# Optimization experiments

Hardware: AMD Instinct MI355X
Metric: run time of the kernel (lower is better)

The kernel has to match this reference:

```python
import jax, jax.numpy as jnp
import numpy as np
import math

EMBED_DIM = 1024
NUM_HEADS = 16
HEAD_DIM = EMBED_DIM // NUM_HEADS  # 64
MAX_SEQ_LEN = 2048


def rope_tables(max_seq_len, dim):
    pos = jnp.arange(max_seq_len, dtype=jnp.float32)
    div_term = jnp.exp(jnp.arange(0, dim, 2, dtype=jnp.float32) * -(math.log(10000.0) / dim))
    ang = pos[:, None] * div_term[None, :]  # [S, dim//2]
    return jnp.sin(ang), jnp.cos(ang)


def apply_rope(x, sin, cos):
    # x: [B, H, S, D]; sin/cos: [max_seq, D//2]
    S = x.shape[2]
    sin = sin[:S][None, None]  # [1,1,S,D//2]
    cos = cos[:S][None, None]
    x1, x2 = jnp.split(x, 2, axis=-1)
    return jnp.concatenate([cos * x1 - sin * x2, sin * x1 + cos * x2], axis=-1)


def setup_inputs() -> dict:
    key = jax.random.key(0)
    ks = jax.random.split(key, 5)
    B, S, E = 4, 2048, EMBED_DIM
    std = 1.0 / math.sqrt(E)
    x = jax.random.normal(ks[0], (B, S, E), dtype=jnp.float32)
    Wq = jax.random.normal(ks[1], (E, E), dtype=jnp.float32) * std
    Wk = jax.random.normal(ks[2], (E, E), dtype=jnp.float32) * std
    Wv = jax.random.normal(ks[3], (E, E), dtype=jnp.float32) * std
    Wo = jax.random.normal(ks[4], (E, E), dtype=jnp.float32) * std
    return {"x": x, "Wq": Wq, "Wk": Wk, "Wv": Wv, "Wo": Wo}


def reference(x, Wq, Wk, Wv, Wo):
    B, S, E = x.shape
    H, D = NUM_HEADS, HEAD_DIM
    scale = 1.0 / math.sqrt(D)
    sin, cos = rope_tables(MAX_SEQ_LEN, D)

    def split_heads(t):
        return t.reshape(B, S, H, D).transpose(0, 2, 1, 3)  # [B,H,S,D]

    q = split_heads(x @ Wq)
    k = split_heads(x @ Wk)
    v = split_heads(x @ Wv)
    q = apply_rope(q, sin, cos)
    k = apply_rope(k, sin, cos)

    scores = jnp.einsum('bhqd,bhkd->bhqk', q, k) * scale
    causal = jnp.where(jnp.tril(jnp.ones((S, S), dtype=bool)), 0.0, -1e9)
    scores = scores + causal[None, None]
    attn = jax.nn.softmax(scores, axis=-1)
    out = jnp.einsum('bhqk,bhkd->bhqd', attn, v)  # [B,H,S,D]
    out = out.transpose(0, 2, 1, 3).reshape(B, S, E)
    return out @ Wo
```

## Files before the change

### kernel.cpp

```cpp
#include <hip/hip_runtime.h>

#define DEVFN __device__ __forceinline__

typedef __attribute__((ext_vector_type(8))) short bf16x8;
typedef __attribute__((ext_vector_type(4))) float f32x4;
typedef __attribute__((ext_vector_type(16))) float f32x16;

#define MFMA16(a, b, c) __builtin_amdgcn_mfma_f32_16x16x32_bf16(a, b, c, 0, 0, 0)
#define MFMA32(a, b, c) __builtin_amdgcn_mfma_f32_32x32x16_bf16(a, b, c, 0, 0, 0)

DEVFN unsigned short f2bf(float f) {
  union { float f; unsigned u; } v; v.f = f;
  unsigned r = v.u + 0x7FFFu + ((v.u >> 16) & 1u);
  return (unsigned short)(r >> 16);
}
DEVFN unsigned pack2bf(float a, float b) {
  return (unsigned)f2bf(a) | ((unsigned)f2bf(b) << 16);
}
DEVFN unsigned cvtpk(float lo, float hi) {
  unsigned r;
  asm("v_cvt_pk_bf16_f32 %0, %1, %2" : "=v"(r) : "v"(lo), "v"(hi));
  return r;
}
DEVFN void pl32swap(unsigned& a, unsigned& b) {
  asm("v_permlane32_swap_b32 %0, %1" : "+v"(a), "+v"(b));
}
DEVFN void gll16(const void* g, void* l) {
  __builtin_amdgcn_global_load_lds((__attribute__((address_space(1))) void*)g,
                                   (__attribute__((address_space(3))) void*)l,
                                   16, 0, 0);
}


__global__ __launch_bounds__(256) void conv_x_k(const float* __restrict__ x,
                                                unsigned short* __restrict__ xb) {
  int i = (blockIdx.x * 256 + threadIdx.x) * 4;
  float4 v = *(const float4*)(x + i);
  uint2 u;
  u.x = pack2bf(v.x, v.y);
  u.y = pack2bf(v.z, v.w);
  *(uint2*)(xb + i) = u;
}

__global__ __launch_bounds__(256) void transp_k(
    const float* __restrict__ Wq, const float* __restrict__ Wk,
    const float* __restrict__ Wv, const float* __restrict__ Wo,
    unsigned short* __restrict__ Tq, unsigned short* __restrict__ Tk,
    unsigned short* __restrict__ Tv, unsigned short* __restrict__ To) {
  __shared__ unsigned short t[64 * 65];
  int z = blockIdx.z;
  const float* src = (z == 0) ? Wq : (z == 1) ? Wk : (z == 2) ? Wv : Wo;
  unsigned short* dst = (z == 0) ? Tq : (z == 1) ? Tk : (z == 2) ? Tv : To;
  int k0 = blockIdx.x * 64, n0 = blockIdx.y * 64;
  int tid = threadIdx.x;
#pragma unroll
  for (int i = 0; i < 16; ++i) {
    int flat = i * 256 + tid;
    int r = flat >> 6, cc = flat & 63;
    t[cc * 65 + r] = f2bf(src[(size_t)(k0 + r) * 1024 + n0 + cc]);
  }
  __syncthreads();
#pragma unroll
  for (int i = 0; i < 16; ++i) {
    int flat = i * 256 + tid;
    int rr = flat >> 6, cc = flat & 63;
    dst[(size_t)(n0 + rr) * 1024 + k0 + cc] = t[rr * 65 + cc];
  }
}

__global__ __launch_bounds__(256) void rope_k(float2* __restrict__ rtab) {
  int idx = blockIdx.x * 256 + threadIdx.x;
  int s = idx >> 5, j = idx & 31;
  float freq = expf(-0.28782313714981824f * (float)j);
  float ang = (float)s * freq;
  rtab[idx] = make_float2(sinf(ang), cosf(ang));
}

__global__ __launch_bounds__(256) void gemm_qkv_k(
    const unsigned short* __restrict__ A, const unsigned short* __restrict__ WTq,
    const unsigned short* __restrict__ WTk, const unsigned short* __restrict__ WTv,
    unsigned short* __restrict__ Qb, unsigned short* __restrict__ Kfb,
    unsigned short* __restrict__ Vfb, const float2* __restrict__ rtab) {
  __shared__ unsigned short At[128 * 64];
  __shared__ unsigned short Bt[128 * 64];
  const int tid = threadIdx.x;
  const int w = tid >> 6, lane = tid & 63, g = lane >> 4, c = lane & 15;
  const int wr = w >> 1, wc = w & 1;
  const int which = blockIdx.y >> 3;
  const unsigned short* WT = (which == 0) ? WTq : (which == 1) ? WTk : WTv;
  const int m0 = blockIdx.x * 128, n0 = (blockIdx.y & 7) * 128;

  f32x4 zero = {0.f, 0.f, 0.f, 0.f};
  f32x4 acc[4][4];
#pragma unroll
  for (int i = 0; i < 4; ++i)
#pragma unroll
    for (int j = 0; j < 4; ++j) acc[i][j] = zero;

  for (int k0 = 0; k0 < 1024; k0 += 64) {
#pragma unroll
    for (int p = 0; p < 4; ++p) {
      int i = p * 256 + tid;
      int row = i >> 3, ls = i & 7;
      size_t off = ((size_t)(m0 + row) * 1024 + k0) * 2 + ((ls ^ (row & 7)) << 4);
      gll16((const char*)A + off, (char*)At + p * 4096 + w * 1024);
      size_t offb = ((size_t)(n0 + row) * 1024 + k0) * 2 + ((ls ^ (row & 7)) << 4);
      gll16((const char*)WT + offb, (char*)Bt + p * 4096 + w * 1024);
    }
    __syncthreads();
#pragma unroll
    for (int ks = 0; ks < 2; ++ks) {
      bf16x8 af[4], bfv[4];
#pragma unroll
      for (int am = 0; am < 4; ++am) {
        int row = wr * 64 + am * 16 + c;
        af[am] = *(const bf16x8*)(At + row * 64 + ((((ks << 2) | g) ^ (row & 7)) << 3));
      }
#pragma unroll
      for (int bn = 0; bn < 4; ++bn) {
        int row = wc * 64 + bn * 16 + c;
        bfv[bn] = *(const bf16x8*)(Bt + row * 64 + ((((ks << 2) | g) ^ (row & 7)) << 3));
      }
#pragma unroll
      for (int am = 0; am < 4; ++am)
#pragma unroll
        for (int bn = 0; bn < 4; ++bn)
          acc[am][bn] = MFMA16(af[am], bfv[bn], acc[am][bn]);
    }
    __syncthreads();
  }

  if (which == 0) {
#pragma unroll
    for (int am = 0; am < 4; ++am)
#pragma unroll
      for (int bp = 0; bp < 2; ++bp) {
        int col = n0 + wc * 64 + bp * 16 + c;
        int h = col >> 6, j = col & 63;
#pragma unroll
        for (int r = 0; r < 4; ++r) {
          int row = m0 + wr * 64 + am * 16 + (g << 2) + r;
          int b = row >> 11, s = row & 2047;
          float x1 = acc[am][bp][r], x2 = acc[am][bp + 2][r];
          float2 sc = rtab[s * 32 + j];
          float o1 = (sc.y * x1 - sc.x * x2) * 0.18033688011112042f;
          float o2 = (sc.x * x1 + sc.y * x2) * 0.18033688011112042f;
          size_t base = (((size_t)(b * 16 + h)) * 2048 + s) * 64;
          Qb[base + j] = f2bf(o1);
          Qb[base + 32 + j] = f2bf(o2);
        }
      }
  } else if (which == 1) {
#pragma unroll
    for (int am = 0; am < 4; ++am)
#pragma unroll
      for (int bp = 0; bp < 2; ++bp) {
        int col = n0 + wc * 64 + bp * 16 + c;
        int h = col >> 6, j = col & 63;
        const int kb = j >> 4, hil = (j >> 3) & 1, el = j & 7;
#pragma unroll
        for (int r = 0; r < 4; ++r) {
          int row = m0 + wr * 64 + am * 16 + (g << 2) + r;
          int b = row >> 11, s = row & 2047;
          float x1 = acc[am][bp][r], x2 = acc[am][bp + 2][r];
          float2 sc = rtab[s * 32 + j];
          float o1 = sc.y * x1 - sc.x * x2;
          float o2 = sc.x * x1 + sc.y * x2;
          size_t base = (size_t)(b * 16 + h) * 131072 + (size_t)(s >> 5) * 2048 +
                        (hil * 32 + (s & 31)) * 8 + el;
          Kfb[base + kb * 512] = f2bf(o1);
          Kfb[base + (kb + 2) * 512] = f2bf(o2);
        }
      }
  } else {
#pragma unroll
    for (int am = 0; am < 4; ++am)
#pragma unroll
      for (int bn = 0; bn < 4; ++bn) {
        int col = n0 + wc * 64 + bn * 16 + c;
        int h = col >> 6, d = col & 63;
        int row0 = m0 + wr * 64 + am * 16 + (g << 2);
        int b = row0 >> 11, s0 = row0 & 2047;
        uint2 u;
        u.x = pack2bf(acc[am][bn][0], acc[am][bn][1]);
        u.y = pack2bf(acc[am][bn][2], acc[am][bn][3]);
        size_t off = (size_t)(b * 16 + h) * 131072 + (size_t)(s0 >> 6) * 4096 +
                     ((s0 >> 4) & 3) * 1024 + (d >> 5) * 512 +
                     (((s0 >> 3) & 1) * 32 + (d & 31)) * 8 + (s0 & 7);
        *(uint2*)(Vfb + off) = u;
      }
  }
}

__global__ __launch_bounds__(256) void gemm_o_k(
    const unsigned short* __restrict__ A, const unsigned short* __restrict__ WT,
    float* __restrict__ outf) {
  __shared__ unsigned short At[128 * 64];
  __shared__ unsigned short Bt[128 * 64];
  const int tid = threadIdx.x;
  const int w = tid >> 6, lane = tid & 63, g = lane >> 4, c = lane & 15;
  const int wr = w >> 1, wc = w & 1;
  const int m0 = blockIdx.x * 128, n0 = blockIdx.y * 128;

  f32x4 zero = {0.f, 0.f, 0.f, 0.f};
  f32x4 acc[4][4];
#pragma unroll
  for (int i = 0; i < 4; ++i)
#pragma unroll
    for (int j = 0; j < 4; ++j) acc[i][j] = zero;

  for (int k0 = 0; k0 < 1024; k0 += 64) {
#pragma unroll
    for (int p = 0; p < 4; ++p) {
      int i = p * 256 + tid;
      int row = i >> 3, ls = i & 7;
      size_t off = ((size_t)(m0 + row) * 1024 + k0) * 2 + ((ls ^ (row & 7)) << 4);
      gll16((const char*)A + off, (char*)At + p * 4096 + w * 1024);
      size_t offb = ((size_t)(n0 + row) * 1024 + k0) * 2 + ((ls ^ (row & 7)) << 4);
      gll16((const char*)WT + offb, (char*)Bt + p * 4096 + w * 1024);
    }
    __syncthreads();
#pragma unroll
    for (int ks = 0; ks < 2; ++ks) {
      bf16x8 af[4], bfv[4];
#pragma unroll
      for (int am = 0; am < 4; ++am) {
        int row = wr * 64 + am * 16 + c;
        af[am] = *(const bf16x8*)(At + row * 64 + ((((ks << 2) | g) ^ (row & 7)) << 3));
      }
#pragma unroll
      for (int bn = 0; bn < 4; ++bn) {
        int row = wc * 64 + bn * 16 + c;
        bfv[bn] = *(const bf16x8*)(Bt + row * 64 + ((((ks << 2) | g) ^ (row & 7)) << 3));
      }
#pragma unroll
      for (int am = 0; am < 4; ++am)
#pragma unroll
        for (int bn = 0; bn < 4; ++bn)
          acc[am][bn] = MFMA16(af[am], bfv[bn], acc[am][bn]);
    }
    __syncthreads();
  }

#pragma unroll
  for (int am = 0; am < 4; ++am)
#pragma unroll
    for (int bn = 0; bn < 4; ++bn)
#pragma unroll
      for (int r = 0; r < 4; ++r)
        outf[(size_t)(m0 + wr * 64 + am * 16 + (g << 2) + r) * 1024 +
             (n0 + wc * 64 + bn * 16 + c)] = acc[am][bn][r];
}

__global__ __launch_bounds__(256, 2) void attn_k(
    const unsigned short* __restrict__ Q, const unsigned short* __restrict__ Kf,
    const unsigned short* __restrict__ Vf, unsigned short* __restrict__ ctx) {
  const int blk = blockIdx.x;
  const int xcd = blk & 7, j = blk >> 3;
  const int hp = j & 3;
  const int s = 31 - (j >> 2);
  const int tid = threadIdx.x;
  const int w = tid >> 6, lane = tid & 63;
  const int hi = lane >> 5, c5 = lane & 31;
  const int bh = xcd * 8 + hp * 2 + (w & 1);
  const int U = 2 * s + (w >> 1);
  const int S = s + 1;
  const int qw = U * 32;

  const unsigned short* Qbh = Q + (size_t)bh * 2048 * 64;
  const unsigned short* Kbh = Kf + (size_t)bh * 131072;
  const unsigned short* Vbh = Vf + (size_t)bh * 131072;
  const int b = bh >> 4, h = bh & 15;

  f32x16 zacc;
#pragma unroll
  for (int i = 0; i < 16; ++i) zacc[i] = 0.f;

  bf16x8 qf[4];
#pragma unroll
  for (int kb = 0; kb < 4; ++kb)
    qf[kb] = *(const bf16x8*)(Qbh + (size_t)(qw + c5) * 64 + kb * 16 + hi * 8);

  f32x16 oacc[2];
  oacc[0] = zacc; oacc[1] = zacc;
  float m_run = -1e30f, l_run = 0.f;

  bf16x8 kfA[2][4], vfA[2][4], kfB[2][4], vfB[2][4];

  auto loadK = [&](int st, bf16x8 (&dst)[2][4]) {
    const unsigned short* kb_ = Kbh + (size_t)st * 4096 + lane * 8;
#pragma unroll
    for (int t = 0; t < 2; ++t)
#pragma unroll
      for (int kb = 0; kb < 4; ++kb)
        dst[t][kb] = *(const bf16x8*)(kb_ + t * 2048 + kb * 512);
  };
  auto loadV = [&](int st, bf16x8 (&dst)[2][4]) {
    const unsigned short* vb_ = Vbh + (size_t)st * 4096 + lane * 8;
#pragma unroll
    for (int kb = 0; kb < 4; ++kb) {
      dst[0][kb] = *(const bf16x8*)(vb_ + kb * 1024);
      dst[1][kb] = *(const bf16x8*)(vb_ + kb * 1024 + 512);
    }
  };

  auto step = [&](int st, bf16x8 (&kfC)[2][4], bf16x8 (&vfC)[2][4],
                  bf16x8 (&kfN)[2][4], bf16x8 (&vfN)[2][4]) {
    f32x16 sacc[2];
    __builtin_amdgcn_s_setprio(1);
#pragma unroll
    for (int t = 0; t < 2; ++t) {
      sacc[t] = MFMA32(kfC[t][0], qf[0], zacc);
#pragma unroll
      for (int kb = 1; kb < 4; ++kb)
        sacc[t] = MFMA32(kfC[t][kb], qf[kb], sacc[t]);
    }
    __builtin_amdgcn_s_setprio(0);

    if (st + 1 < S) {
      loadK(st + 1, kfN);
      loadV(st + 1, vfN);
    }

    if (st == S - 1) {
      const int q = qw + c5;
#pragma unroll
      for (int t = 0; t < 2; ++t) {
        const int kvb = st * 64 + t * 32 + (hi << 2);
#pragma unroll
        for (int i = 0; i < 16; ++i) {
          int kv = kvb + (i & 3) + ((i >> 2) << 3);
          if (kv > q) sacc[t][i] = -1e30f;
        }
      }
    }

    float vmax = fmaxf(sacc[0][0], sacc[0][1]);
#pragma unroll
    for (int t = 0; t < 2; ++t)
#pragma unroll
      for (int i = (t == 0 ? 2 : 0); i < 16; i += 2)
        vmax = fmaxf(vmax, fmaxf(sacc[t][i], sacc[t][i + 1]));
    vmax = fmaxf(vmax, __shfl_xor(vmax, 32, 64));
    if (!__all(vmax <= m_run + 8.0f)) {
      float m_new = fmaxf(m_run, vmax);
      float alpha = exp2f(m_run - m_new);
      l_run *= alpha;
#pragma unroll
      for (int i = 0; i < 16; ++i) {
        oacc[0][i] *= alpha;
        oacc[1][i] *= alpha;
      }
      m_run = m_new;
    }
    float psum = 0.f;
#pragma unroll
    for (int t = 0; t < 2; ++t)
#pragma unroll
      for (int i = 0; i < 16; ++i) {
        float pv = exp2f(sacc[t][i] - m_run);
        sacc[t][i] = pv;
        psum += pv;
      }
    psum += __shfl_xor(psum, 32, 64);
    l_run += psum;

    unsigned pword[4][4];
#pragma unroll
    for (int t = 0; t < 2; ++t) {
      unsigned X[4][2];
#pragma unroll
      for (int u2 = 0; u2 < 4; ++u2)
#pragma unroll
        for (int wp = 0; wp < 2; ++wp)
          X[u2][wp] = cvtpk(sacc[t][u2 * 4 + 2 * wp], sacc[t][u2 * 4 + 2 * wp + 1]);
#pragma unroll
      for (int par = 0; par < 2; ++par) {
        const int kb = 2 * t + par;
#pragma unroll
        for (int wp = 0; wp < 2; ++wp) {
          unsigned a = X[2 * par][wp], b2 = X[2 * par + 1][wp];
          pl32swap(a, b2);
          pword[kb][wp] = a;
          pword[kb][wp + 2] = b2;
        }
      }
    }

    __builtin_amdgcn_s_setprio(1);
#pragma unroll
    for (int kb = 0; kb < 4; ++kb) {
      union { unsigned u[4]; bf16x8 v; } pw;
#pragma unroll
      for (int k2 = 0; k2 < 4; ++k2) pw.u[k2] = pword[kb][k2];
      oacc[0] = MFMA32(vfC[0][kb], pw.v, oacc[0]);
      oacc[1] = MFMA32(vfC[1][kb], pw.v, oacc[1]);
    }
    __builtin_amdgcn_s_setprio(0);
  };

  loadK(0, kfA);
  loadV(0, vfA);
  for (int st = 0; st < S; st += 2) {
    step(st, kfA, vfA, kfB, vfB);
    if (st + 1 < S) step(st + 1, kfB, vfB, kfA, vfA);
  }

  const float linv = 1.f / l_run;
  unsigned short* crow = ctx + ((size_t)(b * 2048 + qw + c5)) * 1024 + h * 64;
#pragma unroll
  for (int dt = 0; dt < 2; ++dt)
#pragma unroll
    for (int u = 0; u < 4; ++u) {
      int d0 = dt * 32 + 8 * u + 4 * hi;
      uint2 o;
      o.x = cvtpk(oacc[dt][4 * u] * linv, oacc[dt][4 * u + 1] * linv);
      o.y = cvtpk(oacc[dt][4 * u + 2] * linv, oacc[dt][4 * u + 3] * linv);
      *(uint2*)(crow + d0) = o;
    }
}


extern "C" void kernel_launch(void* const* d_in, const int* in_sizes, int n_in,
                              void* d_out, int out_size, void* d_ws, size_t ws_size,
                              hipStream_t stream) {
  (void)in_sizes; (void)n_in; (void)out_size; (void)ws_size;
  const float* x = (const float*)d_in[0];
  const float* Wq = (const float*)d_in[1];
  const float* Wk = (const float*)d_in[2];
  const float* Wv = (const float*)d_in[3];
  const float* Wo = (const float*)d_in[4];
  char* ws = (char*)d_ws;
  const size_t MiB = 1024 * 1024;
  unsigned short* xb  = (unsigned short*)(ws);
  unsigned short* WTq = (unsigned short*)(ws + 16 * MiB);
  unsigned short* WTk = (unsigned short*)(ws + 18 * MiB);
  unsigned short* WTv = (unsigned short*)(ws + 20 * MiB);
  unsigned short* WTo = (unsigned short*)(ws + 22 * MiB);
  unsigned short* Qb  = (unsigned short*)(ws + 24 * MiB);
  unsigned short* Kfb = (unsigned short*)(ws + 40 * MiB);
  unsigned short* Vfb = (unsigned short*)(ws + 56 * MiB);
  unsigned short* ctx = (unsigned short*)(ws + 72 * MiB);
  float2* rtab = (float2*)(ws + 88 * MiB);

  conv_x_k<<<8192, 256, 0, stream>>>(x, xb);
  transp_k<<<dim3(16, 16, 4), 256, 0, stream>>>(Wq, Wk, Wv, Wo, WTq, WTk, WTv, WTo);
  rope_k<<<256, 256, 0, stream>>>(rtab);
  gemm_qkv_k<<<dim3(64, 24), 256, 0, stream>>>(xb, WTq, WTk, WTv, Qb, Kfb, Vfb, rtab);
  attn_k<<<1024, 256, 0, stream>>>(Qb, Kfb, Vfb, ctx);
  gemm_o_k<<<dim3(64, 8), 256, 0, stream>>>(ctx, WTo, (float*)d_out);
}
```

Measured before the change: 178.1 us.

## Pair causal query tiles per wave, share K/V loads, and fuse prep kernels

The attention kernel now gives each wave two complementary 32-row query tiles (P and 63-P), so every wave has the same total work under the causal mask, and each K/V tile loaded from memory serves both query tiles. The grid is halved to 512 blocks. The register double-buffering of K/V is replaced by a single buffer: the next K is prefetched while V for the current step is loaded. The max and sum reductions are rewritten as trees. Separately, the conversion, transpose and rope-table kernels are merged into one launch. The trade-offs are higher register pressure from the two accumulator sets, fewer blocks in flight, and less overlap on V loads.

```diff
diff --git a/kernel.cpp b/kernel.cpp
--- a/kernel.cpp
+++ b/kernel.cpp
@@ -31,49 +31,49 @@
                                    16, 0, 0);
 }
 
-
-__global__ __launch_bounds__(256) void conv_x_k(const float* __restrict__ x,
-                                                unsigned short* __restrict__ xb) {
-  int i = (blockIdx.x * 256 + threadIdx.x) * 4;
-  float4 v = *(const float4*)(x + i);
-  uint2 u;
-  u.x = pack2bf(v.x, v.y);
-  u.y = pack2bf(v.z, v.w);
-  *(uint2*)(xb + i) = u;
-}
-
-__global__ __launch_bounds__(256) void transp_k(
+__global__ __launch_bounds__(256) void prep_k(
+    const float* __restrict__ x, unsigned short* __restrict__ xb,
     const float* __restrict__ Wq, const float* __restrict__ Wk,
     const float* __restrict__ Wv, const float* __restrict__ Wo,
     unsigned short* __restrict__ Tq, unsigned short* __restrict__ Tk,
-    unsigned short* __restrict__ Tv, unsigned short* __restrict__ To) {
+    unsigned short* __restrict__ Tv, unsigned short* __restrict__ To,
+    float2* __restrict__ rtab) {
   __shared__ unsigned short t[64 * 65];
-  int z = blockIdx.z;
-  const float* src = (z == 0) ? Wq : (z == 1) ? Wk : (z == 2) ? Wv : Wo;
-  unsigned short* dst = (z == 0) ? Tq : (z == 1) ? Tk : (z == 2) ? Tv : To;
-  int k0 = blockIdx.x * 64, n0 = blockIdx.y * 64;
-  int tid = threadIdx.x;
-#pragma unroll
-  for (int i = 0; i < 16; ++i) {
-    int flat = i * 256 + tid;
-    int r = flat >> 6, cc = flat & 63;
-    t[cc * 65 + r] = f2bf(src[(size_t)(k0 + r) * 1024 + n0 + cc]);
-  }
-  __syncthreads();
-#pragma unroll
-  for (int i = 0; i < 16; ++i) {
-    int flat = i * 256 + tid;
-    int rr = flat >> 6, cc = flat & 63;
-    dst[(size_t)(n0 + rr) * 1024 + k0 + cc] = t[rr * 65 + cc];
-  }
-}
-
-__global__ __launch_bounds__(256) void rope_k(float2* __restrict__ rtab) {
-  int idx = blockIdx.x * 256 + threadIdx.x;
-  int s = idx >> 5, j = idx & 31;
-  float freq = expf(-0.28782313714981824f * (float)j);
-  float ang = (float)s * freq;
-  rtab[idx] = make_float2(sinf(ang), cosf(ang));
+  const int blk = blockIdx.x;
+  const int tid = threadIdx.x;
+  if (blk < 8192) {
+    int i = (blk * 256 + tid) * 4;
+    float4 v = *(const float4*)(x + i);
+    uint2 u;
+    u.x = pack2bf(v.x, v.y);
+    u.y = pack2bf(v.z, v.w);
+    *(uint2*)(xb + i) = u;
+  } else if (blk < 9216) {
+    const int lb = blk - 8192;
+    const int z = lb >> 8, by = (lb >> 4) & 15, bx = lb & 15;
+    const float* src = (z == 0) ? Wq : (z == 1) ? Wk : (z == 2) ? Wv : Wo;
+    unsigned short* dst = (z == 0) ? Tq : (z == 1) ? Tk : (z == 2) ? Tv : To;
+    int k0 = bx * 64, n0 = by * 64;
+#pragma unroll
+    for (int i = 0; i < 16; ++i) {
+      int flat = i * 256 + tid;
+      int r = flat >> 6, cc = flat & 63;
+      t[cc * 65 + r] = f2bf(src[(size_t)(k0 + r) * 1024 + n0 + cc]);
+    }
+    __syncthreads();
+#pragma unroll
+    for (int i = 0; i < 16; ++i) {
+      int flat = i * 256 + tid;
+      int rr = flat >> 6, cc = flat & 63;
+      dst[(size_t)(n0 + rr) * 1024 + k0 + cc] = t[rr * 65 + cc];
+    }
+  } else {
+    int idx = (blk - 9216) * 256 + tid;
+    int s = idx >> 5, j = idx & 31;
+    float freq = expf(-0.28782313714981824f * (float)j);
+    float ang = (float)s * freq;
+    rtab[idx] = make_float2(sinf(ang), cosf(ang));
+  }
 }
 
 __global__ __launch_bounds__(256) void gemm_qkv_k(
@@ -256,16 +256,15 @@
     const unsigned short* __restrict__ Q, const unsigned short* __restrict__ Kf,
     const unsigned short* __restrict__ Vf, unsigned short* __restrict__ ctx) {
   const int blk = blockIdx.x;
-  const int xcd = blk & 7, j = blk >> 3;
-  const int hp = j & 3;
-  const int s = 31 - (j >> 2);
+  const int xcd = blk & 7, idx = blk >> 3;
+  const int bh = (xcd << 3) + (idx & 7);
   const int tid = threadIdx.x;
   const int w = tid >> 6, lane = tid & 63;
   const int hi = lane >> 5, c5 = lane & 31;
-  const int bh = xcd * 8 + hp * 2 + (w & 1);
-  const int U = 2 * s + (w >> 1);
-  const int S = s + 1;
-  const int qw = U * 32;
+  const int P = ((idx >> 3) << 2) + w;
+  const int SA = (P >> 1) + 1;
+  const int SB = ((63 - P) >> 1) + 1;
+  const int qwA = P * 32, qwB = (63 - P) * 32;
 
   const unsigned short* Qbh = Q + (size_t)bh * 2048 * 64;
   const unsigned short* Kbh = Kf + (size_t)bh * 131072;
@@ -276,53 +275,50 @@
 #pragma unroll
   for (int i = 0; i < 16; ++i) zacc[i] = 0.f;
 
-  bf16x8 qf[4];
-#pragma unroll
-  for (int kb = 0; kb < 4; ++kb)
-    qf[kb] = *(const bf16x8*)(Qbh + (size_t)(qw + c5) * 64 + kb * 16 + hi * 8);
-
-  f32x16 oacc[2];
-  oacc[0] = zacc; oacc[1] = zacc;
-  float m_run = -1e30f, l_run = 0.f;
-
-  bf16x8 kfA[2][4], vfA[2][4], kfB[2][4], vfB[2][4];
-
-  auto loadK = [&](int st, bf16x8 (&dst)[2][4]) {
+  bf16x8 qfA[4], qfB[4];
+#pragma unroll
+  for (int kb = 0; kb < 4; ++kb) {
+    qfA[kb] = *(const bf16x8*)(Qbh + (size_t)(qwA + c5) * 64 + kb * 16 + hi * 8);
+    qfB[kb] = *(const bf16x8*)(Qbh + (size_t)(qwB + c5) * 64 + kb * 16 + hi * 8);
+  }
+
+  f32x16 oaccA[2], oaccB[2];
+  oaccA[0] = zacc; oaccA[1] = zacc; oaccB[0] = zacc; oaccB[1] = zacc;
+  float mA = -1e30f, lA = 0.f, mB = -1e30f, lB = 0.f;
+
+  bf16x8 kf[2][4], vf[2][4];
+
+  auto loadK = [&](int st) {
     const unsigned short* kb_ = Kbh + (size_t)st * 4096 + lane * 8;
 #pragma unroll
     for (int t = 0; t < 2; ++t)
 #pragma unroll
       for (int kb = 0; kb < 4; ++kb)
-        dst[t][kb] = *(const bf16x8*)(kb_ + t * 2048 + kb * 512);
-  };
-  auto loadV = [&](int st, bf16x8 (&dst)[2][4]) {
+        kf[t][kb] = *(const bf16x8*)(kb_ + t * 2048 + kb * 512);
+  };
+  auto loadV = [&](int st) {
     const unsigned short* vb_ = Vbh + (size_t)st * 4096 + lane * 8;
 #pragma unroll
     for (int kb = 0; kb < 4; ++kb) {
-      dst[0][kb] = *(const bf16x8*)(vb_ + kb * 1024);
-      dst[1][kb] = *(const bf16x8*)(vb_ + kb * 1024 + 512);
-    }
-  };
-
-  auto step = [&](int st, bf16x8 (&kfC)[2][4], bf16x8 (&vfC)[2][4],
-                  bf16x8 (&kfN)[2][4], bf16x8 (&vfN)[2][4]) {
-    f32x16 sacc[2];
-    __builtin_amdgcn_s_setprio(1);
+      vf[0][kb] = *(const bf16x8*)(vb_ + kb * 1024);
+      vf[1][kb] = *(const bf16x8*)(vb_ + kb * 1024 + 512);
+    }
+  };
+
+  auto qk_unit = [&](const bf16x8 (&qf)[4], f32x16 (&sacc)[2]) {
 #pragma unroll
     for (int t = 0; t < 2; ++t) {
-      sacc[t] = MFMA32(kfC[t][0], qf[0], zacc);
+      sacc[t] = MFMA32(kf[t][0], qf[0], zacc);
 #pragma unroll
       for (int kb = 1; kb < 4; ++kb)
-        sacc[t] = MFMA32(kfC[t][kb], qf[kb], sacc[t]);
-    }
-    __builtin_amdgcn_s_setprio(0);
-
-    if (st + 1 < S) {
-      loadK(st + 1, kfN);
-      loadV(st + 1, vfN);
-    }
-
-    if (st == S - 1) {
+        sacc[t] = MFMA32(kf[t][kb], qf[kb], sacc[t]);
+    }
+  };
+
+  auto sm_unit = [&](f32x16 (&sacc)[2], float& m_run, float& l_run,
+                     f32x16 (&oacc)[2], unsigned (&pword)[4][4], int st,
+                     int Su, int qw) {
+    if (st == Su - 1) {
       const int q = qw + c5;
 #pragma unroll
       for (int t = 0; t < 2; ++t) {
@@ -334,13 +330,15 @@
         }
       }
     }
-
-    float vmax = fmaxf(sacc[0][0], sacc[0][1]);
-#pragma unroll
-    for (int t = 0; t < 2; ++t)
-#pragma unroll
-      for (int i = (t == 0 ? 2 : 0); i < 16; i += 2)
-        vmax = fmaxf(vmax, fmaxf(sacc[t][i], sacc[t][i + 1]));
+    f32x16 mx;
+#pragma unroll
+    for (int i = 0; i < 16; ++i) mx[i] = fmaxf(sacc[0][i], sacc[1][i]);
+    float hx[8];
+#pragma unroll
+    for (int i = 0; i < 8; ++i) hx[i] = fmaxf(mx[i], mx[i + 8]);
+    float q0 = fmaxf(hx[0], hx[4]), q1 = fmaxf(hx[1], hx[5]);
+    float q2 = fmaxf(hx[2], hx[6]), q3 = fmaxf(hx[3], hx[7]);
+    float vmax = fmaxf(fmaxf(q0, q1), fmaxf(q2, q3));
     vmax = fmaxf(vmax, __shfl_xor(vmax, 32, 64));
     if (!__all(vmax <= m_run + 8.0f)) {
       float m_new = fmaxf(m_run, vmax);
@@ -353,19 +351,21 @@
       }
       m_run = m_new;
     }
-    float psum = 0.f;
 #pragma unroll
     for (int t = 0; t < 2; ++t)
 #pragma unroll
-      for (int i = 0; i < 16; ++i) {
-        float pv = exp2f(sacc[t][i] - m_run);
-        sacc[t][i] = pv;
-        psum += pv;
-      }
+      for (int i = 0; i < 16; ++i) sacc[t][i] = exp2f(sacc[t][i] - m_run);
+    f32x16 sm;
+#pragma unroll
+    for (int i = 0; i < 16; ++i) sm[i] = sacc[0][i] + sacc[1][i];
+    float gx[8];
+#pragma unroll
+    for (int i = 0; i < 8; ++i) gx[i] = sm[i] + sm[i + 8];
+    float p0 = gx[0] + gx[4], p1 = gx[1] + gx[5];
+    float p2 = gx[2] + gx[6], p3 = gx[3] + gx[7];
+    float psum = (p0 + p1) + (p2 + p3);
     psum += __shfl_xor(psum, 32, 64);
     l_run += psum;
-
-    unsigned pword[4][4];
 #pragma unroll
     for (int t = 0; t < 2; ++t) {
       unsigned X[4][2];
@@ -386,38 +386,54 @@
         }
       }
     }
-
-    __builtin_amdgcn_s_setprio(1);
+  };
+
+  auto pv_unit = [&](const unsigned (&pword)[4][4], f32x16 (&oacc)[2]) {
 #pragma unroll
     for (int kb = 0; kb < 4; ++kb) {
       union { unsigned u[4]; bf16x8 v; } pw;
 #pragma unroll
       for (int k2 = 0; k2 < 4; ++k2) pw.u[k2] = pword[kb][k2];
-      oacc[0] = MFMA32(vfC[0][kb], pw.v, oacc[0]);
-      oacc[1] = MFMA32(vfC[1][kb], pw.v, oacc[1]);
-    }
+      oacc[0] = MFMA32(vf[0][kb], pw.v, oacc[0]);
+      oacc[1] = MFMA32(vf[1][kb], pw.v, oacc[1]);
+    }
+  };
+
+  loadK(0);
+  for (int st = 0; st < SB; ++st) {
+    const bool actA = (st < SA);
+    f32x16 saccA[2], saccB[2];
+    __builtin_amdgcn_s_setprio(1);
+    if (actA) qk_unit(qfA, saccA);
+    qk_unit(qfB, saccB);
     __builtin_amdgcn_s_setprio(0);
-  };
-
-  loadK(0, kfA);
-  loadV(0, vfA);
-  for (int st = 0; st < S; st += 2) {
-    step(st, kfA, vfA, kfB, vfB);
-    if (st + 1 < S) step(st + 1, kfB, vfB, kfA, vfA);
-  }
-
-  const float linv = 1.f / l_run;
-  unsigned short* crow = ctx + ((size_t)(b * 2048 + qw + c5)) * 1024 + h * 64;
-#pragma unroll
-  for (int dt = 0; dt < 2; ++dt)
-#pragma unroll
-    for (int u = 0; u < 4; ++u) {
-      int d0 = dt * 32 + 8 * u + 4 * hi;
-      uint2 o;
-      o.x = cvtpk(oacc[dt][4 * u] * linv, oacc[dt][4 * u + 1] * linv);
-      o.y = cvtpk(oacc[dt][4 * u + 2] * linv, oacc[dt][4 * u + 3] * linv);
-      *(uint2*)(crow + d0) = o;
-    }
+    if (st + 1 < SB) loadK(st + 1);
+    loadV(st);
+    unsigned pwA[4][4], pwB[4][4];
+    if (actA) sm_unit(saccA, mA, lA, oaccA, pwA, st, SA, qwA);
+    sm_unit(saccB, mB, lB, oaccB, pwB, st, SB, qwB);
+    __builtin_amdgcn_s_setprio(1);
+    if (actA) pv_unit(pwA, oaccA);
+    pv_unit(pwB, oaccB);
+    __builtin_amdgcn_s_setprio(0);
+  }
+
+  auto epi = [&](const f32x16 (&oacc)[2], float l_run, int qw) {
+    const float linv = 1.f / l_run;
+    unsigned short* crow = ctx + ((size_t)(b * 2048 + qw + c5)) * 1024 + h * 64;
+#pragma unroll
+    for (int dt = 0; dt < 2; ++dt)
+#pragma unroll
+      for (int u = 0; u < 4; ++u) {
+        int d0 = dt * 32 + 8 * u + 4 * hi;
+        uint2 o;
+        o.x = cvtpk(oacc[dt][4 * u] * linv, oacc[dt][4 * u + 1] * linv);
+        o.y = cvtpk(oacc[dt][4 * u + 2] * linv, oacc[dt][4 * u + 3] * linv);
+        *(uint2*)(crow + d0) = o;
+      }
+  };
+  epi(oaccA, lA, qwA);
+  epi(oaccB, lB, qwB);
 }
 
 
@@ -443,10 +459,8 @@
   unsigned short* ctx = (unsigned short*)(ws + 72 * MiB);
   float2* rtab = (float2*)(ws + 88 * MiB);
 
-  conv_x_k<<<8192, 256, 0, stream>>>(x, xb);
-  transp_k<<<dim3(16, 16, 4), 256, 0, stream>>>(Wq, Wk, Wv, Wo, WTq, WTk, WTv, WTo);
-  rope_k<<<256, 256, 0, stream>>>(rtab);
+  prep_k<<<9472, 256, 0, stream>>>(x, xb, Wq, Wk, Wv, Wo, WTq, WTk, WTv, WTo, rtab);
   gemm_qkv_k<<<dim3(64, 24), 256, 0, stream>>>(xb, WTq, WTk, WTv, Qb, Kfb, Vfb, rtab);
-  attn_k<<<1024, 256, 0, stream>>>(Qb, Kfb, Vfb, ctx);
+  attn_k<<<512, 256, 0, stream>>>(Qb, Kfb, Vfb, ctx);
   gemm_o_k<<<dim3(64, 8), 256, 0, stream>>>(ctx, WTo, (float*)d_out);
 }
```

Result: slower. 181.8 us (+2.1%).
